# Kernel optimization log

Measured on AMD Instinct MI355X. Metric: run time of the kernel, lower is better.

## Reference

```python
import jax, jax.numpy as jnp
import numpy as np

NEG_SLOPE = 0.2
EPS = 1e-10

B, N, F_IN = 2, 20000, 128
H, D = 4, 32
E = 640000


def setup_inputs() -> dict:
    key = jax.random.key(0)
    k1, k2, k3, k4, k5 = jax.random.split(key, 5)
    x = jax.random.normal(k1, (B, N, F_IN), dtype=jnp.float32)
    edge_index = jax.random.randint(k2, (2, E), 0, N, dtype=jnp.int64)
    W = jax.random.normal(k3, (H * D, F_IN), dtype=jnp.float32) * (1.0 / np.sqrt(F_IN))
    a_src = jax.random.normal(k4, (H, D), dtype=jnp.float32) * (1.0 / np.sqrt(D))
    a_dst = jax.random.normal(k5, (H, D), dtype=jnp.float32) * (1.0 / np.sqrt(D))
    return {"x": x, "edge_index": edge_index, "W": W, "a_src": a_src, "a_dst": a_dst}


def reference(x, edge_index, W, a_src, a_dst):
    # x: (B, N, F_IN); edge_index: (2, E); W: (H*D, F_IN)
    Bs, Ns, _ = x.shape
    h = (x @ W.T).reshape(Bs, Ns, H, D)          # (B, N, H, D)
    src = edge_index[0]
    dst = edge_index[1]

    h_src = h[:, src]                            # (B, E, H, D) gather
    e_src = jnp.einsum('behd,hd->beh', h_src, a_src)
    e_dst = jnp.einsum('behd,hd->beh', h[:, dst], a_dst)
    e = jax.nn.leaky_relu(e_src + e_dst, NEG_SLOPE)  # (B, E, H)

    # segment softmax over destination nodes (segments on leading axis)
    e_t = jnp.moveaxis(e, 1, 0)                  # (E, B, H)
    max_n = jax.ops.segment_max(e_t, dst, num_segments=Ns)   # (N, B, H)
    exp_e = jnp.exp(e_t - max_n[dst])            # (E, B, H)
    sum_n = jax.ops.segment_sum(exp_e, dst, num_segments=Ns)  # (N, B, H)
    alpha = exp_e / (sum_n[dst] + EPS)           # (E, B, H)

    messages = alpha[..., None] * jnp.moveaxis(h_src, 1, 0)  # (E, B, H, D)
    out = jax.ops.segment_sum(messages, dst, num_segments=Ns)  # (N, B, H, D)
    out = jnp.moveaxis(out, 0, 1).reshape(Bs, Ns, H * D)       # concat heads
    return out
```

## Files before the change

### kernel.cpp

```cpp
#include <hip/hip_runtime.h>
#include <math.h>

#define N_NODES 20000
#define N_B 2
#define N_H 4
#define N_D 32
#define N_F 128
#define N_E 640000
#define BNH (N_B * N_NODES * N_H)

#define GEMM_BLOCKS 625
#define P1_BLOCKS 250
#define EPB 2560
#define NBINS 157
#define NODE_CAP 96
#define TRS 136
#define LOG2E 1.44269504088896f

typedef __attribute__((ext_vector_type(8))) short short8v;
typedef __attribute__((ext_vector_type(4))) float floatx4;

__device__ __forceinline__ unsigned short f2bf(float f) {
  unsigned u = __float_as_uint(f);
  return (unsigned short)((u + 0x7FFFu + ((u >> 16) & 1u)) >> 16);
}

__global__ __launch_bounds__(256) void fused_gemm_p1(
    const float* __restrict__ X, const float* __restrict__ W,
    const int* __restrict__ EI, const float* __restrict__ a_src,
    const float* __restrict__ a_dst, unsigned short* __restrict__ HbI,
    float* __restrict__ sI, float* __restrict__ sdI,
    int* __restrict__ cntB, int* __restrict__ prefB,
    unsigned* __restrict__ blockEdges) {
  __shared__ union {
    struct {
      unsigned short WbS[128 * 128];
      unsigned short Tr[4][16 * TRS];
    } g;
    struct {
      int hist[NBINS];
      int pref[NBINS];
      int wsum[4];
      unsigned buf[EPB];
    } p;
  } sm;
  const int tid = threadIdx.x;

  if (blockIdx.x >= GEMM_BLOCKS) {
    const int pb = blockIdx.x - GEMM_BLOCKS;
    const int e0 = pb * EPB;
    for (int t = tid; t < NBINS; t += 256) sm.p.hist[t] = 0;
    __syncthreads();
    for (int k = 0; k < EPB; k += 256) {
      const int d = EI[N_E + e0 + k + tid];
      atomicAdd(&sm.p.hist[d >> 7], 1);
    }
    __syncthreads();
    {
      const int w = tid >> 6, lane = tid & 63;
      int v = 0, incl = 0;
      if (tid < NBINS) v = sm.p.hist[tid];
      if (w < 3) {
        incl = v;
#pragma unroll
        for (int off = 1; off < 64; off <<= 1) {
          int t2 = __shfl_up(incl, off);
          if (lane >= off) incl += t2;
        }
        if (lane == 63) sm.p.wsum[w] = incl;
      }
      __syncthreads();
      if (tid < NBINS) {
        int add = 0;
        if (w >= 1) add += sm.p.wsum[0];
        if (w >= 2) add += sm.p.wsum[1];
        sm.p.pref[tid] = incl - v + add;
      }
      __syncthreads();
    }
    for (int t = tid; t < NBINS; t += 256) {
      cntB[pb * NBINS + t] = sm.p.hist[t];
      prefB[pb * NBINS + t] = sm.p.pref[t];
      sm.p.hist[t] = sm.p.pref[t];
    }
    __syncthreads();
    for (int k = 0; k < EPB; k += 256) {
      const int i = e0 + k + tid;
      const int d = EI[N_E + i];
      const int s = EI[i];
      const int pos = atomicAdd(&sm.p.hist[d >> 7], 1);
      sm.p.buf[pos] = (unsigned)(((d & 127) << 16) | s);
    }
    __syncthreads();
    for (int k = tid; k < EPB; k += 256)
      blockEdges[(size_t)pb * EPB + k] = sm.p.buf[k];
    return;
  }

  {
    const int o = tid >> 1;
    const int khalf = (tid & 1) * 64;
#pragma unroll
    for (int c = 0; c < 8; ++c) {
      const int k0 = khalf + c * 8;
      const float4 w0 = *(const float4*)&W[(size_t)o * 128 + k0];
      const float4 w1 = *(const float4*)&W[(size_t)o * 128 + k0 + 4];
      union { unsigned short us[8]; uint4 v; } pk;
      pk.us[0] = f2bf(w0.x); pk.us[1] = f2bf(w0.y);
      pk.us[2] = f2bf(w0.z); pk.us[3] = f2bf(w0.w);
      pk.us[4] = f2bf(w1.x); pk.us[5] = f2bf(w1.y);
      pk.us[6] = f2bf(w1.z); pk.us[7] = f2bf(w1.w);
      const int chunk = (k0 >> 3) ^ (o & 15);
      *(uint4*)&sm.g.WbS[o * 128 + chunk * 8] = pk.v;
    }
  }
  __syncthreads();

  const int wv = tid >> 6, lane = tid & 63;
  const int l15 = lane & 15;
  const int row0 = blockIdx.x * 64 + wv * 16;
  const int arow = row0 + l15;
  const int kg = lane >> 4;

  float as[8], ad[8];
#pragma unroll
  for (int cf = 0; cf < 8; ++cf) {
    as[cf] = a_src[cf * 16 + l15];
    ad[cf] = a_dst[cf * 16 + l15];
  }

  short8v afr[4];
#pragma unroll
  for (int kc = 0; kc < 4; ++kc) {
    const size_t xb = (size_t)arow * 128 + kc * 32 + kg * 8;
    const float4 x0 = *(const float4*)&X[xb];
    const float4 x1 = *(const float4*)&X[xb + 4];
    afr[kc][0] = (short)f2bf(x0.x); afr[kc][1] = (short)f2bf(x0.y);
    afr[kc][2] = (short)f2bf(x0.z); afr[kc][3] = (short)f2bf(x0.w);
    afr[kc][4] = (short)f2bf(x1.x); afr[kc][5] = (short)f2bf(x1.y);
    afr[kc][6] = (short)f2bf(x1.z); afr[kc][7] = (short)f2bf(x1.w);
  }

  floatx4 acc[8];
#pragma unroll
  for (int cf = 0; cf < 8; ++cf) acc[cf] = (floatx4){0.f, 0.f, 0.f, 0.f};

#pragma unroll
  for (int kc = 0; kc < 4; ++kc) {
#pragma unroll
    for (int cf = 0; cf < 8; ++cf) {
      const int o = cf * 16 + l15;
      const int chunk = (kc * 4 + kg) ^ l15;
      const short8v bfr = *(const short8v*)&sm.g.WbS[o * 128 + chunk * 8];
      acc[cf] = __builtin_amdgcn_mfma_f32_16x16x32_bf16(afr[kc], bfr, acc[cf], 0, 0, 0);
    }
  }

  {
    float ps[4][4], pd[4][4];
#pragma unroll
    for (int j = 0; j < 4; ++j)
#pragma unroll
      for (int h = 0; h < 4; ++h) {
        float vs = acc[2 * h][j] * as[2 * h] + acc[2 * h + 1][j] * as[2 * h + 1];
        float vd = acc[2 * h][j] * ad[2 * h] + acc[2 * h + 1][j] * ad[2 * h + 1];
#pragma unroll
        for (int m = 1; m <= 8; m <<= 1) {
          vs += __shfl_xor(vs, m);
          vd += __shfl_xor(vd, m);
        }
        ps[j][h] = vs * LOG2E; pd[j][h] = vd * LOG2E;
      }
    if (l15 == 0) {
#pragma unroll
      for (int j = 0; j < 4; ++j) {
        const int m = row0 + kg * 4 + j;
        const int node = (m < N_NODES) ? m : m - N_NODES;
        const int boff = (m < N_NODES) ? 0 : 4;
#pragma unroll
        for (int h = 0; h < 4; ++h) {
          sI[node * 8 + boff + h] = ps[j][h];
          sdI[node * 8 + boff + h] = pd[j][h];
        }
      }
    }
  }

#pragma unroll
  for (int cf = 0; cf < 8; ++cf)
#pragma unroll
    for (int j = 0; j < 4; ++j)
      sm.g.Tr[wv][((kg << 2) + j) * TRS + cf * 16 + l15] = f2bf(acc[cf][j]);
#pragma unroll
  for (int it = 0; it < 4; ++it) {
    const int r = it * 4 + kg;
    const int m = row0 + r;
    const size_t base2 =
        (m < N_NODES) ? (size_t)m * 256 : (size_t)(m - N_NODES) * 256 + 128;
    const uint4 v = *(const uint4*)&sm.g.Tr[wv][r * TRS + l15 * 8];
    *(uint4*)&HbI[base2 + l15 * 8] = v;
  }
}

__global__ __launch_bounds__(256) void bin_kernel(
    const unsigned* __restrict__ blockEdges, const int* __restrict__ cntB,
    const int* __restrict__ prefB, unsigned short* __restrict__ bucket,
    int* __restrict__ count) {
  __shared__ unsigned short list[128][NODE_CAP];
  __shared__ int cnt[128];
  const int bin = blockIdx.x;
  const int tid = threadIdx.x;
  if (tid < 128) cnt[tid] = 0;
  __syncthreads();
  for (int b = tid; b < P1_BLOCKS; b += 256) {
    const int c = cntB[b * NBINS + bin];
    const int p0 = prefB[b * NBINS + bin];
    const size_t base = (size_t)b * EPB + p0;
    for (int q = 0; q < c; ++q) {
      const unsigned u = blockEdges[base + q];
      const int dl = (int)(u >> 16);
      const int r = atomicAdd(&cnt[dl], 1);
      if (r < NODE_CAP) list[dl][r] = (unsigned short)(u & 0xFFFFu);
    }
  }
  __syncthreads();
  const int dl = tid >> 1, half = tid & 1;
  const int node = bin * 128 + dl;
  if (node < N_NODES) {
    const int c = min(cnt[dl], NODE_CAP);
    if (half == 0) count[node] = c;
#pragma unroll
    for (int q = 0; q < 6; ++q) {
      const int off = (half * 6 + q) * 8;
      if (off < c)
        *(uint4*)&bucket[(size_t)node * NODE_CAP + off] =
            *(const uint4*)&list[dl][off];
    }
  }
}

__global__ __launch_bounds__(256) void agg_kernel(
    const uint4* __restrict__ Hu4, const float* __restrict__ sI,
    const float* __restrict__ sdI, const int* __restrict__ count,
    const unsigned short* __restrict__ bucket, float* __restrict__ out) {
  const int s = blockIdx.x & 3;
  const int wv = threadIdx.x >> 6;
  const int node = (blockIdx.x >> 2) * 4 + wv;
  const int lane = threadIdx.x & 63;
  const int eq = lane >> 3;
  const int fl = lane & 7;
  const int j = (8 * s + fl) >> 2;
  const int hoff = 8 * s + fl;

  const int cnt = count[node];
  const float sd = sdI[node * 8 + j];
  const int bbase = node * NODE_CAP;

  float den = 0.f;
  float acc[8];
#pragma unroll
  for (int k = 0; k < 8; ++k) acc[k] = 0.f;

  for (int cb = 0; cb < cnt; cb += 64) {
    const int c = min(cnt - cb, 64);
    const int vE = (lane < c) ? (int)bucket[bbase + cb + lane] : 0;
    for (int e = 0; e < c; e += 8) {
      const int idx = e + eq;
      const bool v = idx < c;
      const int src = __shfl(vE, v ? idx : 0);
      const uint4 h = Hu4[((unsigned)src << 5) + hoff];
      float lg = sI[src * 8 + j] + sd;
      lg = fmaxf(lg, 0.2f * lg);
      const float p = v ? exp2f(lg) : 0.f;
      den += p;
      acc[0] = fmaf(p, __uint_as_float(h.x << 16), acc[0]);
      acc[1] = fmaf(p, __uint_as_float(h.x & 0xFFFF0000u), acc[1]);
      acc[2] = fmaf(p, __uint_as_float(h.y << 16), acc[2]);
      acc[3] = fmaf(p, __uint_as_float(h.y & 0xFFFF0000u), acc[3]);
      acc[4] = fmaf(p, __uint_as_float(h.z << 16), acc[4]);
      acc[5] = fmaf(p, __uint_as_float(h.z & 0xFFFF0000u), acc[5]);
      acc[6] = fmaf(p, __uint_as_float(h.w << 16), acc[6]);
      acc[7] = fmaf(p, __uint_as_float(h.w & 0xFFFF0000u), acc[7]);
    }
  }

#pragma unroll
  for (int m = 8; m <= 32; m <<= 1) {
    den += __shfl_xor(den, m);
#pragma unroll
    for (int k = 0; k < 8; ++k) acc[k] += __shfl_xor(acc[k], m);
  }

  if (lane < 8) {
    const float inv = 1.f / (den + 1e-10f);
    const int i0 = 64 * s + 8 * fl;
    const int b = i0 >> 7, f0 = i0 & 127;
    float4 o0, o1;
    o0.x = acc[0] * inv; o0.y = acc[1] * inv;
    o0.z = acc[2] * inv; o0.w = acc[3] * inv;
    o1.x = acc[4] * inv; o1.y = acc[5] * inv;
    o1.z = acc[6] * inv; o1.w = acc[7] * inv;
    float* op = &out[(size_t)b * (N_NODES * 128) + (size_t)node * 128 + f0];
    *(float4*)op = o0;
    *(float4*)(op + 4) = o1;
  }
}

extern "C" void kernel_launch(void* const* d_in, const int* in_sizes, int n_in,
                              void* d_out, int out_size, void* d_ws, size_t ws_size,
                              hipStream_t stream) {
  const float* X = (const float*)d_in[0];
  const int* EI = (const int*)d_in[1];
  const float* W = (const float*)d_in[2];
  const float* a_src = (const float*)d_in[3];
  const float* a_dst = (const float*)d_in[4];
  float* out = (float*)d_out;

  unsigned short* hbI = (unsigned short*)d_ws;
  float* sI = (float*)(hbI + (size_t)N_B * N_NODES * N_F);
  float* sdI = sI + BNH;
  int* cntB = (int*)(sdI + BNH);
  int* prefB = cntB + P1_BLOCKS * NBINS;
  unsigned* blockEdges = (unsigned*)(prefB + P1_BLOCKS * NBINS);
  int* count = (int*)(blockEdges + (size_t)N_E);
  unsigned short* bucket = (unsigned short*)(count + N_NODES);

  fused_gemm_p1<<<GEMM_BLOCKS + P1_BLOCKS, 256, 0, stream>>>(
      X, W, EI, a_src, a_dst, hbI, sI, sdI, cntB, prefB, blockEdges);
  bin_kernel<<<NBINS, 256, 0, stream>>>(blockEdges, cntB, prefB, bucket, count);
  agg_kernel<<<(N_NODES / 4) * 4, 256, 0, stream>>>(
      (const uint4*)hbI, sI, sdI, count, bucket, out);
}
```

Baseline: 79.18 us.

## Precompute per-edge attention weights in separate kernel before aggregation

Adds a p_kernel that computes the leaky-relu and exp2 attention weight for every bucket slot and all 8 batch-head planes, storing them as bf16 in a planar buffer. The aggregation kernel then reads the precomputed weight plus the source index directly instead of doing a gather of sI, the exp, and the shuffle-based index broadcast. This takes exp and the sI gathers off the latency-bound aggregation loop, but adds a kernel launch, extra global traffic (about 30 MB of bf16 weights written and read back), and rounds the weights to bf16.

```diff
diff --git a/kernel.cpp b/kernel.cpp
--- a/kernel.cpp
+++ b/kernel.cpp
@@ -14,6 +14,7 @@
 #define EPB 2560
 #define NBINS 157
 #define NODE_CAP 96
+#define NSLOTS (N_NODES * NODE_CAP)
 #define TRS 136
 #define LOG2E 1.44269504088896f
 
@@ -239,49 +240,69 @@
   }
 }
 
+__global__ __launch_bounds__(256) void p_kernel(
+    const unsigned short* __restrict__ bucket, const int* __restrict__ count,
+    const float* __restrict__ sI, const float* __restrict__ sdI,
+    unsigned short* __restrict__ pS) {
+  const int f = blockIdx.x * 256 + threadIdx.x;
+  const int node = f / NODE_CAP;
+  const int e = f - node * NODE_CAP;
+  const int cnt = count[node];
+  const bool v = e < cnt;
+  const int src = v ? (int)bucket[f] : 0;
+  const float4 si0 = *(const float4*)&sI[src * 8];
+  const float4 si1 = *(const float4*)&sI[src * 8 + 4];
+  const float4 sd0 = *(const float4*)&sdI[node * 8];
+  const float4 sd1 = *(const float4*)&sdI[node * 8 + 4];
+  float lg[8];
+  lg[0] = si0.x + sd0.x; lg[1] = si0.y + sd0.y;
+  lg[2] = si0.z + sd0.z; lg[3] = si0.w + sd0.w;
+  lg[4] = si1.x + sd1.x; lg[5] = si1.y + sd1.y;
+  lg[6] = si1.z + sd1.z; lg[7] = si1.w + sd1.w;
+#pragma unroll
+  for (int j = 0; j < 8; ++j) {
+    float l = fmaxf(lg[j], 0.2f * lg[j]);
+    const float p = v ? exp2f(l) : 0.f;
+    pS[(unsigned)j * NSLOTS + f] = f2bf(p);
+  }
+}
+
 __global__ __launch_bounds__(256) void agg_kernel(
-    const uint4* __restrict__ Hu4, const float* __restrict__ sI,
-    const float* __restrict__ sdI, const int* __restrict__ count,
-    const unsigned short* __restrict__ bucket, float* __restrict__ out) {
+    const uint4* __restrict__ Hu4, const unsigned short* __restrict__ bucket,
+    const unsigned short* __restrict__ pS, const int* __restrict__ count,
+    float* __restrict__ out) {
   const int s = blockIdx.x & 3;
   const int wv = threadIdx.x >> 6;
   const int node = (blockIdx.x >> 2) * 4 + wv;
   const int lane = threadIdx.x & 63;
   const int eq = lane >> 3;
   const int fl = lane & 7;
-  const int j = (8 * s + fl) >> 2;
   const int hoff = 8 * s + fl;
+  const unsigned jplane = (unsigned)(2 * s + (fl >> 2));
 
   const int cnt = count[node];
-  const float sd = sdI[node * 8 + j];
   const int bbase = node * NODE_CAP;
+  const unsigned pbase = jplane * (unsigned)NSLOTS + (unsigned)bbase;
 
   float den = 0.f;
   float acc[8];
 #pragma unroll
   for (int k = 0; k < 8; ++k) acc[k] = 0.f;
 
-  for (int cb = 0; cb < cnt; cb += 64) {
-    const int c = min(cnt - cb, 64);
-    const int vE = (lane < c) ? (int)bucket[bbase + cb + lane] : 0;
-    for (int e = 0; e < c; e += 8) {
-      const int idx = e + eq;
-      const bool v = idx < c;
-      const int src = __shfl(vE, v ? idx : 0);
-      const uint4 h = Hu4[((unsigned)src << 5) + hoff];
-      float lg = sI[src * 8 + j] + sd;
-      lg = fmaxf(lg, 0.2f * lg);
-      const float p = v ? exp2f(lg) : 0.f;
-      den += p;
-      acc[0] = fmaf(p, __uint_as_float(h.x << 16), acc[0]);
-      acc[1] = fmaf(p, __uint_as_float(h.x & 0xFFFF0000u), acc[1]);
-      acc[2] = fmaf(p, __uint_as_float(h.y << 16), acc[2]);
-      acc[3] = fmaf(p, __uint_as_float(h.y & 0xFFFF0000u), acc[3]);
-      acc[4] = fmaf(p, __uint_as_float(h.z << 16), acc[4]);
-      acc[5] = fmaf(p, __uint_as_float(h.z & 0xFFFF0000u), acc[5]);
-      acc[6] = fmaf(p, __uint_as_float(h.w << 16), acc[6]);
-      acc[7] = fmaf(p, __uint_as_float(h.w & 0xFFFF0000u), acc[7]);
-    }
+  for (int e = eq; e < cnt; e += 8) {
+    const int src = (int)bucket[bbase + e];
+    const float p =
+        __uint_as_float((unsigned)pS[pbase + (unsigned)e] << 16);
+    const uint4 h = Hu4[((unsigned)src << 5) + hoff];
+    den += p;
+    acc[0] = fmaf(p, __uint_as_float(h.x << 16), acc[0]);
+    acc[1] = fmaf(p, __uint_as_float(h.x & 0xFFFF0000u), acc[1]);
+    acc[2] = fmaf(p, __uint_as_float(h.y << 16), acc[2]);
+    acc[3] = fmaf(p, __uint_as_float(h.y & 0xFFFF0000u), acc[3]);
+    acc[4] = fmaf(p, __uint_as_float(h.z << 16), acc[4]);
+    acc[5] = fmaf(p, __uint_as_float(h.z & 0xFFFF0000u), acc[5]);
+    acc[6] = fmaf(p, __uint_as_float(h.w << 16), acc[6]);
+    acc[7] = fmaf(p, __uint_as_float(h.w & 0xFFFF0000u), acc[7]);
   }
 
 #pragma unroll
@@ -324,10 +345,12 @@
   unsigned* blockEdges = (unsigned*)(prefB + P1_BLOCKS * NBINS);
   int* count = (int*)(blockEdges + (size_t)N_E);
   unsigned short* bucket = (unsigned short*)(count + N_NODES);
+  unsigned short* pS = bucket + (size_t)NSLOTS;
 
   fused_gemm_p1<<<GEMM_BLOCKS + P1_BLOCKS, 256, 0, stream>>>(
       X, W, EI, a_src, a_dst, hbI, sI, sdI, cntB, prefB, blockEdges);
   bin_kernel<<<NBINS, 256, 0, stream>>>(blockEdges, cntB, prefB, bucket, count);
+  p_kernel<<<NSLOTS / 256, 256, 0, stream>>>(bucket, count, sI, sdI, pS);
   agg_kernel<<<(N_NODES / 4) * 4, 256, 0, stream>>>(
-      (const uint4*)hbI, sI, sdI, count, bucket, out);
-}
+      (const uint4*)hbI, bucket, pS, count, out);
+}
```

New measurement: 94.00 us. 18.7% more time.
